# Kernel tuning notes

Hardware: AMD Instinct MI355X
Metric: run time of the kernel (lower is better)

## Reference

```python
import jax, jax.numpy as jnp
import numpy as np

A = 180      # number of projection angles (theta = arange(180))
STEPS = 4    # partial-sum bands -> output has 1+STEPS channels


def _radon(x):
    # x: [N, 1, W, W]
    N, C, H, W = x.shape
    img = x[:, 0]  # [N, W, W]

    # --- affine grids for all angles (torch affine_grid, align_corners=False) ---
    thetas = jnp.arange(A, dtype=jnp.float32) * (jnp.pi / 180.0)
    c = jnp.cos(thetas)[:, None, None]   # [A,1,1]
    s = jnp.sin(thetas)[:, None, None]
    # align_corners=False base coords: centers of pixels in [-1, 1]
    base = ((jnp.arange(W, dtype=jnp.float32) + 0.5) * (2.0 / W)) - 1.0
    bx = base[None, None, :]             # [1,1,W] (x varies along last dim)
    by = base[None, :, None]             # [1,W,1] (y varies along rows)
    # R = [[cos, sin, 0], [-sin, cos, 0]]
    gx = c * bx + s * by                 # [A,W,W] normalized sample x
    gy = -s * bx + c * by                # [A,W,W] normalized sample y

    # --- bilinear grid_sample, padding_mode='zeros', align_corners=False ---
    ix = ((gx + 1.0) * W - 1.0) * 0.5
    iy = ((gy + 1.0) * W - 1.0) * 0.5
    x0 = jnp.floor(ix).astype(jnp.int32); x1 = x0 + 1
    y0 = jnp.floor(iy).astype(jnp.int32); y1 = y0 + 1
    wx1 = ix - x0; wx0 = 1.0 - wx1
    wy1 = iy - y0; wy0 = 1.0 - wy1

    def gather(yy, xx, w):
        valid = ((yy >= 0) & (yy < W) & (xx >= 0) & (xx < W)).astype(img.dtype)
        v = img[:, jnp.clip(yy, 0, W - 1), jnp.clip(xx, 0, W - 1)]  # [N,A,W,W]
        return v * (valid * w)[None]

    sampled = (gather(y0, x0, wy0 * wx0) + gather(y0, x1, wy0 * wx1)
               + gather(y1, x0, wy1 * wx0) + gather(y1, x1, wy1 * wx1))  # [N,A,W,W]

    # --- normalized hard masks: band of rows |row - center| < t, divided by band size ---
    segs = np.linspace(1, W / 2, STEPS + 1, dtype=int)
    ran = np.abs(np.arange(W) - (W - 1) / 2.0)
    wts = np.stack([(ran < t).astype(np.float32) / max((ran < t).sum(), 1)
                    for t in segs])  # [1+STEPS, W]

    # out[n, s, w, a] = sum_h sampled[n, a, h, w] * wts[s, h]
    return jnp.einsum('nahw,sh->nswa', sampled, jnp.asarray(wts))


def setup_inputs() -> dict:
    key = jax.random.key(0)
    x = jax.random.normal(key, (4, 1, 256, 256), dtype=jnp.float32)
    return {"x": x}


def reference(x):
    return _radon(x)
```

## Files before the change

### kernel.cpp

```cpp
#include <hip/hip_runtime.h>


constexpr int WIDTH  = 256;
constexpr int NANG   = 180;
constexpr int NBATCH = 4;
constexpr int NS     = 5;
constexpr int LSTR   = 270;
constexpr int ROWS   = 260;

__device__ inline unsigned pack2_f16(float a, float b) {
    _Float16 ha = (_Float16)a, hb = (_Float16)b;
    unsigned short ua = __builtin_bit_cast(unsigned short, ha);
    unsigned short ub = __builtin_bit_cast(unsigned short, hb);
    return (unsigned)ua | ((unsigned)ub << 16);
}

__global__ __launch_bounds__(1024) void radon_kernel(const float* __restrict__ x,
                                                     float* __restrict__ out) {
    __shared__ _Float16 lds[ROWS * LSTR];

    const int blk = blockIdx.x;
    const int n = blk / NANG;
    const int a = blk - n * NANG;
    const int t = threadIdx.x;
    const int w = t & 255;
    const int quarter = t >> 8;

    const float* __restrict__ img = x + (size_t)n * WIDTH * WIDTH;

    const float theta = (float)a * 0.017453292519943295f;
    float s, c;
    sincosf(theta, &s, &c);
    const bool transp = (c * c > s * s);

    unsigned* l32 = (unsigned*)lds;
    for (int i = t; i < ROWS * LSTR / 2; i += 1024) l32[i] = 0u;
    __syncthreads();

    if (!transp) {
        for (int d = t; d < 32768; d += 1024) {
            const int y = d >> 7, xd = d & 127;
            const float2 v = ((const float2*)img)[d];
            *(unsigned*)&lds[(y + 2) * LSTR + 2 * xd + 2] = pack2_f16(v.x, v.y);
        }
    } else {
        for (int yp = quarter; yp < 128; yp += 4) {
            const int y = 2 * yp;
            const float v0 = img[y * WIDTH + w];
            const float v1 = img[y * WIDTH + WIDTH + w];
            *(unsigned*)&lds[(w + 2) * LSTR + y + 2] = pack2_f16(v0, v1);
        }
    }
    __syncthreads();

    const float bw  = ((float)w + 0.5f) * (2.0f / WIDTH) - 1.0f;
    const float bh0 = 0.5f * (2.0f / WIDTH) - 1.0f;
    const float gx0 = c * bw + s * bh0;
    const float gy0 = -s * bw + c * bh0;
    const float ix0 = ((gx0 + 1.0f) * (float)WIDTH - 1.0f) * 0.5f;
    const float iy0 = ((gy0 + 1.0f) * (float)WIDTH - 1.0f) * 0.5f;

    const float fast0 = (transp ? iy0 : ix0) + 2.0f;
    const float slow0 = (transp ? ix0 : iy0) + 2.0f;
    const float dfast = transp ? c : s;
    const float dslow = transp ? s : c;

    float r0 = 0.f, r1 = 0.f, r2 = 0.f, r3 = 0.f, r4 = 0.f;

    auto sample = [&](int h, float& r) {
        float fa = fmaf((float)h, dfast, fast0);
        float sl = fmaf((float)h, dslow, slow0);
        fa = __builtin_amdgcn_fmed3f(fa, 1.0f, 258.0f);
        sl = __builtin_amdgcn_fmed3f(sl, 1.0f, 258.0f);
        const float ff = floorf(fa), fs = floorf(sl);
        const float wf1 = fa - ff, wf0 = 1.0f - wf1;
        const float ws1 = sl - fs, ws0 = 1.0f - ws1;
        const int fi = (int)ff, si = (int)fs;
        const _Float16* p = &lds[si * LSTR + fi];
        const float v00 = (float)p[0];
        const float v01 = (float)p[1];
        const float v10 = (float)p[LSTR];
        const float v11 = (float)p[LSTR + 1];
        const float row0 = fmaf(wf1, v01, wf0 * v00);
        const float row1 = fmaf(wf1, v11, wf0 * v10);
        r = fmaf(ws0, row0, r);
        r = fmaf(ws1, row1, r);
    };

    if (quarter == 0) {
        #pragma unroll 8
        for (int h = 0; h < 32; ++h)    sample(h, r4);
        #pragma unroll 8
        for (int h = 32; h < 64; ++h)   sample(h, r3);
    } else if (quarter == 1) {
        #pragma unroll 8
        for (int h = 64; h < 96; ++h)   sample(h, r2);
        #pragma unroll 8
        for (int h = 96; h < 127; ++h)  sample(h, r1);
        sample(127, r0);
    } else if (quarter == 2) {
        sample(128, r0);
        #pragma unroll 8
        for (int h = 129; h < 160; ++h) sample(h, r1);
        #pragma unroll 8
        for (int h = 160; h < 192; ++h) sample(h, r2);
    } else {
        #pragma unroll 8
        for (int h = 192; h < 224; ++h) sample(h, r3);
        #pragma unroll 8
        for (int h = 224; h < 256; ++h) sample(h, r4);
    }

    __syncthreads();
    float* red = (float*)lds;
    const int base = t * NS;
    red[base + 0] = r0;
    red[base + 1] = r1;
    red[base + 2] = r2;
    red[base + 3] = r3;
    red[base + 4] = r4;
    __syncthreads();

    if (t < 256) {
        const int b0 = t * NS, b1 = b0 + 256 * NS, b2 = b0 + 512 * NS, b3 = b0 + 768 * NS;
        const float s0 = (red[b0+0] + red[b1+0]) + (red[b2+0] + red[b3+0]);
        const float s1 = (red[b0+1] + red[b1+1]) + (red[b2+1] + red[b3+1]);
        const float s2 = (red[b0+2] + red[b1+2]) + (red[b2+2] + red[b3+2]);
        const float s3 = (red[b0+3] + red[b1+3]) + (red[b2+3] + red[b3+3]);
        const float s4 = (red[b0+4] + red[b1+4]) + (red[b2+4] + red[b3+4]);

        float* o = out + (((size_t)n * NS) * WIDTH + (size_t)t) * NANG + (size_t)a;
        float cum = s0;
        o[0]                          = cum * (1.0f / 2.0f);
        cum += s1;
        o[(size_t)1 * WIDTH * NANG]   = cum * (1.0f / 64.0f);
        cum += s2;
        o[(size_t)2 * WIDTH * NANG]   = cum * (1.0f / 128.0f);
        cum += s3;
        o[(size_t)3 * WIDTH * NANG]   = cum * (1.0f / 192.0f);
        cum += s4;
        o[(size_t)4 * WIDTH * NANG]   = cum * (1.0f / 256.0f);
    }
}

extern "C" void kernel_launch(void* const* d_in, const int* in_sizes, int n_in,
                              void* d_out, int out_size, void* d_ws, size_t ws_size,
                              hipStream_t stream) {
    const float* x = (const float*)d_in[0];
    float* out = (float*)d_out;
    radon_kernel<<<NBATCH * NANG, 1024, 0, stream>>>(x, out);
}
```

Before: 60.98 us.

## Interleave rows across quarter-waves, remap block order, and simplify bilinear lerp

```diff
diff --git a/kernel.cpp b/kernel.cpp
--- a/kernel.cpp
+++ b/kernel.cpp
@@ -19,12 +19,13 @@
                                                      float* __restrict__ out) {
     __shared__ _Float16 lds[ROWS * LSTR];
 
-    const int blk = blockIdx.x;
-    const int n = blk / NANG;
-    const int a = blk - n * NANG;
+    const int bid = blockIdx.x;
+    const int lin = (bid & 7) * 90 + (bid >> 3);
+    const int n = lin / NANG;
+    const int a = lin - n * NANG;
     const int t = threadIdx.x;
     const int w = t & 255;
-    const int quarter = t >> 8;
+    const int q = t >> 8;
 
     const float* __restrict__ img = x + (size_t)n * WIDTH * WIDTH;
 
@@ -44,7 +45,7 @@
             *(unsigned*)&lds[(y + 2) * LSTR + 2 * xd + 2] = pack2_f16(v.x, v.y);
         }
     } else {
-        for (int yp = quarter; yp < 128; yp += 4) {
+        for (int yp = q; yp < 128; yp += 4) {
             const int y = 2 * yp;
             const float v0 = img[y * WIDTH + w];
             const float v1 = img[y * WIDTH + WIDTH + w];
@@ -67,49 +68,49 @@
 
     float r0 = 0.f, r1 = 0.f, r2 = 0.f, r3 = 0.f, r4 = 0.f;
 
-    auto sample = [&](int h, float& r) {
-        float fa = fmaf((float)h, dfast, fast0);
-        float sl = fmaf((float)h, dslow, slow0);
+    auto sample = [&](int h) -> float {
+        const float hf = (float)h;
+        float fa = fmaf(hf, dfast, fast0);
+        float sl = fmaf(hf, dslow, slow0);
         fa = __builtin_amdgcn_fmed3f(fa, 1.0f, 258.0f);
         sl = __builtin_amdgcn_fmed3f(sl, 1.0f, 258.0f);
         const float ff = floorf(fa), fs = floorf(sl);
-        const float wf1 = fa - ff, wf0 = 1.0f - wf1;
-        const float ws1 = sl - fs, ws0 = 1.0f - ws1;
+        const float wf = fa - ff, ws = sl - fs;
         const int fi = (int)ff, si = (int)fs;
         const _Float16* p = &lds[si * LSTR + fi];
         const float v00 = (float)p[0];
         const float v01 = (float)p[1];
         const float v10 = (float)p[LSTR];
         const float v11 = (float)p[LSTR + 1];
-        const float row0 = fmaf(wf1, v01, wf0 * v00);
-        const float row1 = fmaf(wf1, v11, wf0 * v10);
-        r = fmaf(ws0, row0, r);
-        r = fmaf(ws1, row1, r);
+        const float row0 = fmaf(wf, v01 - v00, v00);
+        const float row1 = fmaf(wf, v11 - v10, v10);
+        return fmaf(ws, row1 - row0, row0);
     };
 
-    if (quarter == 0) {
-        #pragma unroll 8
-        for (int h = 0; h < 32; ++h)    sample(h, r4);
-        #pragma unroll 8
-        for (int h = 32; h < 64; ++h)   sample(h, r3);
-    } else if (quarter == 1) {
-        #pragma unroll 8
-        for (int h = 64; h < 96; ++h)   sample(h, r2);
-        #pragma unroll 8
-        for (int h = 96; h < 127; ++h)  sample(h, r1);
-        sample(127, r0);
-    } else if (quarter == 2) {
-        sample(128, r0);
-        #pragma unroll 8
-        for (int h = 129; h < 160; ++h) sample(h, r1);
-        #pragma unroll 8
-        for (int h = 160; h < 192; ++h) sample(h, r2);
-    } else {
-        #pragma unroll 8
-        for (int h = 192; h < 224; ++h) sample(h, r3);
-        #pragma unroll 8
-        for (int h = 224; h < 256; ++h) sample(h, r4);
+    #pragma unroll
+    for (int k = 0; k < 8; ++k) r4 += sample(q + 4 * k);
+    #pragma unroll
+    for (int k = 0; k < 8; ++k) r3 += sample(32 + q + 4 * k);
+    #pragma unroll
+    for (int k = 0; k < 8; ++k) r2 += sample(64 + q + 4 * k);
+    #pragma unroll
+    for (int k = 0; k < 8; ++k) {
+        const int h = 96 + q + 4 * k;
+        const float v = sample(h);
+        if (h == 127) r0 += v; else r1 += v;
     }
+    #pragma unroll
+    for (int k = 0; k < 8; ++k) {
+        const int h = 128 + q + 4 * k;
+        const float v = sample(h);
+        if (h == 128) r0 += v; else r1 += v;
+    }
+    #pragma unroll
+    for (int k = 0; k < 8; ++k) r2 += sample(160 + q + 4 * k);
+    #pragma unroll
+    for (int k = 0; k < 8; ++k) r3 += sample(192 + q + 4 * k);
+    #pragma unroll
+    for (int k = 0; k < 8; ++k) r4 += sample(224 + q + 4 * k);
 
     __syncthreads();
     float* red = (float*)lds;
```

New measurement: 182.3 us. 199% more time.

## Store image as packed f16 pairs in LDS, use dword loads, swizzle block order

Applied to the files above, without the earlier changes.

```diff
diff --git a/kernel.cpp b/kernel.cpp
--- a/kernel.cpp
+++ b/kernel.cpp
@@ -5,7 +5,7 @@
 constexpr int NANG   = 180;
 constexpr int NBATCH = 4;
 constexpr int NS     = 5;
-constexpr int LSTR   = 270;
+constexpr int CSTR   = 131;
 constexpr int ROWS   = 260;
 
 __device__ inline unsigned pack2_f16(float a, float b) {
@@ -17,11 +17,12 @@
 
 __global__ __launch_bounds__(1024) void radon_kernel(const float* __restrict__ x,
                                                      float* __restrict__ out) {
-    __shared__ _Float16 lds[ROWS * LSTR];
+    __shared__ unsigned cells[ROWS * CSTR];
 
-    const int blk = blockIdx.x;
-    const int n = blk / NANG;
-    const int a = blk - n * NANG;
+    const int bid = blockIdx.x;
+    const int lin = (bid & 7) * 90 + (bid >> 3);
+    const int n = lin / NANG;
+    const int a = lin - n * NANG;
     const int t = threadIdx.x;
     const int w = t & 255;
     const int quarter = t >> 8;
@@ -33,22 +34,20 @@
     sincosf(theta, &s, &c);
     const bool transp = (c * c > s * s);
 
-    unsigned* l32 = (unsigned*)lds;
-    for (int i = t; i < ROWS * LSTR / 2; i += 1024) l32[i] = 0u;
+    for (int i = t; i < ROWS * CSTR; i += 1024) cells[i] = 0u;
     __syncthreads();
 
     if (!transp) {
         for (int d = t; d < 32768; d += 1024) {
             const int y = d >> 7, xd = d & 127;
             const float2 v = ((const float2*)img)[d];
-            *(unsigned*)&lds[(y + 2) * LSTR + 2 * xd + 2] = pack2_f16(v.x, v.y);
+            cells[(y + 2) * CSTR + xd + 1] = pack2_f16(v.x, v.y);
         }
     } else {
         for (int yp = quarter; yp < 128; yp += 4) {
-            const int y = 2 * yp;
-            const float v0 = img[y * WIDTH + w];
-            const float v1 = img[y * WIDTH + WIDTH + w];
-            *(unsigned*)&lds[(w + 2) * LSTR + y + 2] = pack2_f16(v0, v1);
+            const float v0 = img[(2 * yp) * WIDTH + w];
+            const float v1 = img[(2 * yp + 1) * WIDTH + w];
+            cells[(w + 2) * CSTR + yp + 1] = pack2_f16(v0, v1);
         }
     }
     __syncthreads();
@@ -68,51 +67,82 @@
     float r0 = 0.f, r1 = 0.f, r2 = 0.f, r3 = 0.f, r4 = 0.f;
 
     auto sample = [&](int h, float& r) {
-        float fa = fmaf((float)h, dfast, fast0);
-        float sl = fmaf((float)h, dslow, slow0);
+        const float hf = (float)h;
+        float fa = fmaf(hf, dfast, fast0);
+        float sl = fmaf(hf, dslow, slow0);
         fa = __builtin_amdgcn_fmed3f(fa, 1.0f, 258.0f);
         sl = __builtin_amdgcn_fmed3f(sl, 1.0f, 258.0f);
         const float ff = floorf(fa), fs = floorf(sl);
-        const float wf1 = fa - ff, wf0 = 1.0f - wf1;
-        const float ws1 = sl - fs, ws0 = 1.0f - ws1;
+        const float wf = fa - ff, ws = sl - fs;
         const int fi = (int)ff, si = (int)fs;
-        const _Float16* p = &lds[si * LSTR + fi];
-        const float v00 = (float)p[0];
-        const float v01 = (float)p[1];
-        const float v10 = (float)p[LSTR];
-        const float v11 = (float)p[LSTR + 1];
-        const float row0 = fmaf(wf1, v01, wf0 * v00);
-        const float row1 = fmaf(wf1, v11, wf0 * v10);
-        r = fmaf(ws0, row0, r);
-        r = fmaf(ws1, row1, r);
+        const int j = fi >> 1;
+        const int sh = (fi & 1) << 4;
+        const unsigned* rowA = &cells[si * CSTR + j];
+        const unsigned loA = rowA[0],    hiA = rowA[1];
+        const unsigned loB = rowA[CSTR], hiB = rowA[CSTR + 1];
+        const unsigned pairA = (unsigned)(((((unsigned long long)hiA) << 32) | loA) >> sh);
+        const unsigned pairB = (unsigned)(((((unsigned long long)hiB) << 32) | loB) >> sh);
+        const float v00 = (float)__builtin_bit_cast(_Float16, (unsigned short)pairA);
+        const float v01 = (float)__builtin_bit_cast(_Float16, (unsigned short)(pairA >> 16));
+        const float v10 = (float)__builtin_bit_cast(_Float16, (unsigned short)pairB);
+        const float v11 = (float)__builtin_bit_cast(_Float16, (unsigned short)(pairB >> 16));
+        const float row0 = fmaf(wf, v01 - v00, v00);
+        const float row1 = fmaf(wf, v11 - v10, v10);
+        r = fmaf(ws, row1 - row0, r + 0.0f * row0), r = fmaf(ws, row1 - row0, row0) + r - fmaf(ws, row1 - row0, row0) + fmaf(ws, row1 - row0, row0);
     };
+
+    auto sample2 = [&](int h, float& r) {
+        const float hf = (float)h;
+        float fa = fmaf(hf, dfast, fast0);
+        float sl = fmaf(hf, dslow, slow0);
+        fa = __builtin_amdgcn_fmed3f(fa, 1.0f, 258.0f);
+        sl = __builtin_amdgcn_fmed3f(sl, 1.0f, 258.0f);
+        const float ff = floorf(fa), fs = floorf(sl);
+        const float wf = fa - ff, ws = sl - fs;
+        const int fi = (int)ff, si = (int)fs;
+        const int j = fi >> 1;
+        const int sh = (fi & 1) << 4;
+        const unsigned* rowA = &cells[si * CSTR + j];
+        const unsigned loA = rowA[0],    hiA = rowA[1];
+        const unsigned loB = rowA[CSTR], hiB = rowA[CSTR + 1];
+        const unsigned pairA = (unsigned)(((((unsigned long long)hiA) << 32) | loA) >> sh);
+        const unsigned pairB = (unsigned)(((((unsigned long long)hiB) << 32) | loB) >> sh);
+        const float v00 = (float)__builtin_bit_cast(_Float16, (unsigned short)pairA);
+        const float v01 = (float)__builtin_bit_cast(_Float16, (unsigned short)(pairA >> 16));
+        const float v10 = (float)__builtin_bit_cast(_Float16, (unsigned short)pairB);
+        const float v11 = (float)__builtin_bit_cast(_Float16, (unsigned short)(pairB >> 16));
+        const float row0 = fmaf(wf, v01 - v00, v00);
+        const float row1 = fmaf(wf, v11 - v10, v10);
+        r += fmaf(ws, row1 - row0, row0);
+    };
+    (void)sample;
 
     if (quarter == 0) {
         #pragma unroll 8
-        for (int h = 0; h < 32; ++h)    sample(h, r4);
+        for (int h = 0; h < 32; ++h)    sample2(h, r4);
         #pragma unroll 8
-        for (int h = 32; h < 64; ++h)   sample(h, r3);
+        for (int h = 32; h < 64; ++h)   sample2(h, r3);
     } else if (quarter == 1) {
         #pragma unroll 8
-        for (int h = 64; h < 96; ++h)   sample(h, r2);
+        for (int h = 64; h < 96; ++h)   sample2(h, r2);
         #pragma unroll 8
-        for (int h = 96; h < 127; ++h)  sample(h, r1);
-        sample(127, r0);
+        for (int h = 96; h < 127; ++h)  sample2(h, r1);
+        sample2(127, r0);
     } else if (quarter == 2) {
-        sample(128, r0);
+        sample2(128, r0);
         #pragma unroll 8
-        for (int h = 129; h < 160; ++h) sample(h, r1);
+        for (int h = 129; h < 160; ++h) sample2(h, r1);
         #pragma unroll 8
-        for (int h = 160; h < 192; ++h) sample(h, r2);
+        for (int h = 160; h < 192; ++h) sample2(h, r2);
     } else {
         #pragma unroll 8
-        for (int h = 192; h < 224; ++h) sample(h, r3);
+        for (int h = 192; h < 224; ++h) sample2(h, r3);
         #pragma unroll 8
-        for (int h = 224; h < 256; ++h) sample(h, r4);
+        for (int h = 224; h < 256; ++h) sample2(h, r4);
     }
 
     __syncthreads();
-    float* red = (float*)lds;
+    float* red = (float*)cells;
     const int base = t * NS;
     red[base + 0] = r0;
     red[base + 1] = r1;
```

Result: faster. 58.04 us (-4.8%).

## Pack LDS as f16 pairs, use alignbit fetch and packed-half bilinear interpolation

Applied to the files above, without the earlier changes.

```diff
diff --git a/kernel.cpp b/kernel.cpp
--- a/kernel.cpp
+++ b/kernel.cpp
@@ -5,8 +5,16 @@
 constexpr int NANG   = 180;
 constexpr int NBATCH = 4;
 constexpr int NS     = 5;
-constexpr int LSTR   = 270;
+constexpr int CSTR   = 131;
 constexpr int ROWS   = 260;
+
+typedef _Float16 h2 __attribute__((ext_vector_type(2)));
+
+#if __has_builtin(__builtin_amdgcn_fractf)
+#define FRACT(x) __builtin_amdgcn_fractf(x)
+#else
+#define FRACT(x) ((x) - floorf(x))
+#endif
 
 __device__ inline unsigned pack2_f16(float a, float b) {
     _Float16 ha = (_Float16)a, hb = (_Float16)b;
@@ -17,11 +25,12 @@
 
 __global__ __launch_bounds__(1024) void radon_kernel(const float* __restrict__ x,
                                                      float* __restrict__ out) {
-    __shared__ _Float16 lds[ROWS * LSTR];
+    __shared__ unsigned cells[ROWS * CSTR];
 
-    const int blk = blockIdx.x;
-    const int n = blk / NANG;
-    const int a = blk - n * NANG;
+    const int bid = blockIdx.x;
+    const int lin = (bid & 7) * 90 + (bid >> 3);
+    const int n = lin / NANG;
+    const int a = lin - n * NANG;
     const int t = threadIdx.x;
     const int w = t & 255;
     const int quarter = t >> 8;
@@ -33,22 +42,27 @@
     sincosf(theta, &s, &c);
     const bool transp = (c * c > s * s);
 
-    unsigned* l32 = (unsigned*)lds;
-    for (int i = t; i < ROWS * LSTR / 2; i += 1024) l32[i] = 0u;
+    for (int i = t; i < 2 * CSTR; i += 1024) {
+        cells[i] = 0u;
+        cells[258 * CSTR + i] = 0u;
+    }
+    if (t < ROWS) {
+        const int b = t * CSTR;
+        cells[b] = 0u; cells[b + 129] = 0u; cells[b + 130] = 0u;
+    }
     __syncthreads();
 
     if (!transp) {
         for (int d = t; d < 32768; d += 1024) {
             const int y = d >> 7, xd = d & 127;
             const float2 v = ((const float2*)img)[d];
-            *(unsigned*)&lds[(y + 2) * LSTR + 2 * xd + 2] = pack2_f16(v.x, v.y);
+            cells[(y + 2) * CSTR + xd + 1] = pack2_f16(v.x, v.y);
         }
     } else {
         for (int yp = quarter; yp < 128; yp += 4) {
-            const int y = 2 * yp;
-            const float v0 = img[y * WIDTH + w];
-            const float v1 = img[y * WIDTH + WIDTH + w];
-            *(unsigned*)&lds[(w + 2) * LSTR + y + 2] = pack2_f16(v0, v1);
+            const float v0 = img[(2 * yp) * WIDTH + w];
+            const float v1 = img[(2 * yp + 1) * WIDTH + w];
+            cells[(w + 2) * CSTR + yp + 1] = pack2_f16(v0, v1);
         }
     }
     __syncthreads();
@@ -68,23 +82,29 @@
     float r0 = 0.f, r1 = 0.f, r2 = 0.f, r3 = 0.f, r4 = 0.f;
 
     auto sample = [&](int h, float& r) {
-        float fa = fmaf((float)h, dfast, fast0);
-        float sl = fmaf((float)h, dslow, slow0);
+        const float hf = (float)h;
+        float fa = fmaf(hf, dfast, fast0);
+        float sl = fmaf(hf, dslow, slow0);
         fa = __builtin_amdgcn_fmed3f(fa, 1.0f, 258.0f);
         sl = __builtin_amdgcn_fmed3f(sl, 1.0f, 258.0f);
-        const float ff = floorf(fa), fs = floorf(sl);
-        const float wf1 = fa - ff, wf0 = 1.0f - wf1;
-        const float ws1 = sl - fs, ws0 = 1.0f - ws1;
-        const int fi = (int)ff, si = (int)fs;
-        const _Float16* p = &lds[si * LSTR + fi];
-        const float v00 = (float)p[0];
-        const float v01 = (float)p[1];
-        const float v10 = (float)p[LSTR];
-        const float v11 = (float)p[LSTR + 1];
-        const float row0 = fmaf(wf1, v01, wf0 * v00);
-        const float row1 = fmaf(wf1, v11, wf0 * v10);
-        r = fmaf(ws0, row0, r);
-        r = fmaf(ws1, row1, r);
+        const int fi = (int)fa, si = (int)sl;
+        const float wf = FRACT(fa);
+        const float ws = FRACT(sl);
+        const int j = fi >> 1;
+        const int sh = (fi & 1) << 4;
+        const unsigned* rowA = &cells[__mul24(si, CSTR) + j];
+        const unsigned loA = rowA[0],    hiA = rowA[1];
+        const unsigned loB = rowA[CSTR], hiB = rowA[CSTR + 1];
+        const unsigned pa = __builtin_amdgcn_alignbit(hiA, loA, sh);
+        const unsigned pb = __builtin_amdgcn_alignbit(hiB, loB, sh);
+        const h2 va = __builtin_bit_cast(h2, pa);
+        const h2 vb = __builtin_bit_cast(h2, pb);
+        const _Float16 wsh = (_Float16)ws;
+        const h2 ws2 = {wsh, wsh};
+        const h2 col = (vb - va) * ws2 + va;
+        const float c0 = (float)col.x;
+        const float c1 = (float)col.y;
+        r += fmaf(wf, c1 - c0, c0);
     };
 
     if (quarter == 0) {
@@ -112,7 +132,7 @@
     }
 
     __syncthreads();
-    float* red = (float*)lds;
+    float* red = (float*)cells;
     const int base = t * NS;
     red[base + 0] = r0;
     red[base + 1] = r1;
```

Result: faster. 51.41 us (-15.7%).
